# Optimization experiments

Measured on AMD Instinct MI355X. Metric: run time of the kernel, lower is better.

## Reference

```python
import jax, jax.numpy as jnp
import numpy as np

B, C, L, CH, CW = 2, 8, 512, 256, 8
NH = 8
FEATURES = 256
ROT = FEATURES // NH  # 32, partial rotary dim


def _rope(x, rot_dim):
    # x: (..., l, hd); rotate first rot_dim dims (interleaved pairs), pass rest through
    l = x.shape[-2]
    inv_freq = 1.0 / (10000.0 ** (jnp.arange(0, rot_dim, 2, dtype=jnp.float32) / rot_dim))
    freqs = jnp.arange(l, dtype=jnp.float32)[:, None] * inv_freq[None, :]  # (l, rot/2)
    freqs = jnp.repeat(freqs, 2, axis=-1)  # (l, rot)
    cos, sin = jnp.cos(freqs), jnp.sin(freqs)
    xr, xp = x[..., :rot_dim], x[..., rot_dim:]
    x2 = xr.reshape(xr.shape[:-1] + (rot_dim // 2, 2))
    rot = jnp.stack((-x2[..., 1], x2[..., 0]), axis=-1).reshape(xr.shape)
    return jnp.concatenate([xr * cos + rot * sin, xp], axis=-1)


def _conv(z, w):
    return jax.lax.conv_general_dilated(z, w, (1, 1), ((1, 1), (1, 1)),
                                        dimension_numbers=('NCHW', 'OIHW', 'NCHW'))


def _mlin(z, w):
    # per-channel linear over the height (features) axis: (n,c,h,w) x (c,g,h) -> (n,c,g,w)
    return jnp.einsum('nchw,cgh->ncgw', z, w)


def setup_inputs() -> dict:
    key = jax.random.key(0)
    ks = jax.random.split(key, 10)
    s_conv = 1.0 / np.sqrt(C * 9)
    s_lin = 1.0 / np.sqrt(FEATURES)
    return {
        'x': jax.random.normal(ks[0], (B, C, L, CH, CW), jnp.float32),
        'prev_qk': jax.random.normal(ks[1], (B, C, NH, L, L), jnp.float32),
        'conv_q_w': jax.random.normal(ks[2], (C, C, 3, 3), jnp.float32) * s_conv,
        'conv_k_w': jax.random.normal(ks[3], (C, C, 3, 3), jnp.float32) * s_conv,
        'conv_v_w': jax.random.normal(ks[4], (C, C, 3, 3), jnp.float32) * s_conv,
        'wq': jax.random.normal(ks[5], (C, FEATURES, FEATURES), jnp.float32) * s_lin,
        'wk': jax.random.normal(ks[6], (C, FEATURES, FEATURES), jnp.float32) * s_lin,
        'wv': jax.random.normal(ks[7], (C, FEATURES, FEATURES), jnp.float32) * s_lin,
        'wo': jax.random.normal(ks[8], (C, FEATURES, FEATURES), jnp.float32) * s_lin,
    }


def reference(x, prev_qk, conv_q_w, conv_k_w, conv_v_w, wq, wk, wv, wo):
    b, c, l, ch, cw = x.shape
    h = x.transpose(0, 2, 1, 3, 4).reshape(b * l, c, ch, cw)

    def heads(z):  # (b*l,c,ch,cw) -> (b,c,NH,l,hd)
        return (z.reshape(b, l, c, ch * cw).transpose(0, 2, 1, 3)
                 .reshape(b, c, l, NH, -1).transpose(0, 1, 3, 2, 4))

    q = heads(_mlin(_conv(h, conv_q_w), wq))
    k = heads(_mlin(_conv(h, conv_k_w), wk))
    v = heads(_mlin(_conv(h, conv_v_w), wv))

    q = _rope(q, ROT)
    k = _rope(k, ROT)

    qk = jnp.einsum('bcnld,bcnmd->bcnlm', q, k) / jnp.sqrt(jnp.float32(ch)) + prev_qk
    a = jnp.einsum('bcnlm,bcnmd->bcnld', jax.nn.softmax(qk, axis=-1), v)
    a = a.transpose(0, 1, 3, 2, 4).reshape(b, c, l, ch, cw)

    out = (_mlin(a.transpose(0, 2, 1, 3, 4).reshape(b * l, c, ch, cw), wo)
           .reshape(b, l, c, ch, cw).transpose(0, 2, 1, 3, 4))
    return out, qk
```

## Files before the change

### kernel.cpp

```cpp
#include <hip/hip_runtime.h>
#include <cstddef>
#include <cstdint>


typedef unsigned short u16;
typedef unsigned int u32;
typedef __attribute__((ext_vector_type(8))) short short8;
typedef __attribute__((ext_vector_type(4))) float floatx4;

__device__ __forceinline__ float bf2f(u16 u) {
  union { u32 i; float f; } v; v.i = ((u32)u) << 16; return v.f;
}
__device__ __forceinline__ u16 f2bf(float f) {
  union { float f; u32 i; } v; v.f = f;
  return (u16)((v.i + 0x7fffu + ((v.i >> 16) & 1u)) >> 16);
}

__global__ __launch_bounds__(256) void convert_w_kernel(
    const float* __restrict__ wq, const float* __restrict__ wk,
    const float* __restrict__ wv, const float* __restrict__ wo,
    u16* __restrict__ wbf) {
  int mat = blockIdx.y;
  const float* src = (mat == 0) ? wq : (mat == 1) ? wk : (mat == 2) ? wv : wo;
  int idx = blockIdx.x * 256 + threadIdx.x;
  wbf[(size_t)mat * 524288 + idx] = f2bf(src[idx]);
}

__global__ __launch_bounds__(256) void conv_fused_kernel(
    const float* __restrict__ x,
    const float* __restrict__ wq, const float* __restrict__ wk,
    const float* __restrict__ wv,
    u16* __restrict__ oq, u16* __restrict__ ok, u16* __restrict__ ov) {
  __shared__ float wl[1728];
  int t = threadIdx.x;
  for (int i2 = t; i2 < 1728; i2 += 256)
    wl[i2] = (i2 < 576) ? wq[i2] : (i2 < 1152 ? wk[i2 - 576] : wv[i2 - 1152]);
  __syncthreads();

  int bl = blockIdx.x >> 1, ih = blockIdx.x & 1;
  int b = bl >> 9, l = bl & 511;
  int il = t & 127, sh = t >> 7;
  int i = ih * 128 + il;

  float acc[12][8];
#pragma unroll
  for (int p = 0; p < 12; ++p)
#pragma unroll
    for (int j = 0; j < 8; ++j) acc[p][j] = 0.f;

  for (int ci = 0; ci < 8; ++ci) {
    const float* xc = x + (((size_t)(b * 8 + ci) * 512 + l) << 11);
    float xr[3][10];
#pragma unroll
    for (int di = 0; di < 3; ++di) {
      int gi = i + di - 1;
      xr[di][0] = 0.f; xr[di][9] = 0.f;
      if (gi >= 0 && gi < 256) {
        float4 a = *(const float4*)(xc + gi * 8);
        float4 bq = *(const float4*)(xc + gi * 8 + 4);
        xr[di][1] = a.x; xr[di][2] = a.y; xr[di][3] = a.z; xr[di][4] = a.w;
        xr[di][5] = bq.x; xr[di][6] = bq.y; xr[di][7] = bq.z; xr[di][8] = bq.w;
      } else {
#pragma unroll
        for (int j = 1; j < 9; ++j) xr[di][j] = 0.f;
      }
    }
#pragma unroll
    for (int p = 0; p < 12; ++p) {
      int pp = sh * 12 + p;
      int s = pp >> 3, co = pp & 7;
      const float* wp = &wl[s * 576 + (co * 8 + ci) * 9];
      float w00 = wp[0], w01 = wp[1], w02 = wp[2];
      float w10 = wp[3], w11 = wp[4], w12 = wp[5];
      float w20 = wp[6], w21 = wp[7], w22 = wp[8];
#pragma unroll
      for (int j = 0; j < 8; ++j) {
        acc[p][j] += w00 * xr[0][j] + w01 * xr[0][j + 1] + w02 * xr[0][j + 2]
                   + w10 * xr[1][j] + w11 * xr[1][j + 1] + w12 * xr[1][j + 2]
                   + w20 * xr[2][j] + w21 * xr[2][j + 1] + w22 * xr[2][j + 2];
      }
    }
  }
#pragma unroll
  for (int p = 0; p < 12; ++p) {
    int pp = sh * 12 + p;
    int s = pp >> 3, co = pp & 7;
    u16* ob = (s == 0) ? oq : (s == 1) ? ok : ov;
    size_t base = ((size_t)(bl * 8 + co)) << 11;
#pragma unroll
    for (int j = 0; j < 8; ++j) ob[base + j * 256 + i] = f2bf(acc[p][j]);
  }
}

template <int MODE>
__global__ __launch_bounds__(256) void mlin_mfma_kernel(
    const u16* __restrict__ zin,
    const u16* __restrict__ wbf,
    void* __restrict__ outp) {
  __shared__ u16 lds_a[8192];
  __shared__ u16 lds_b[8192];

  int tid = threadIdx.x;
  int wv = tid >> 6, lane = tid & 63;
  int fn = lane & 15, fq = lane >> 4;
  int wr = wv & 1, wc = wv >> 1;

  int bx = blockIdx.x;
  int c = bx >> 7;
  int cblk = (bx >> 1) & 63;
  int gblk = bx & 1;
  int g0 = gblk * 128;
  int col0 = cblk * 128;

  const u16* wsrc = wbf + ((size_t)c << 16);

  floatx4 acc[4][4];
#pragma unroll
  for (int mf = 0; mf < 4; ++mf)
#pragma unroll
    for (int nf = 0; nf < 4; ++nf) acc[mf][nf] = (floatx4){0.f, 0.f, 0.f, 0.f};

  for (int kt = 0; kt < 4; ++kt) {
    int h0 = kt * 64;
#pragma unroll
    for (int it = 0; it < 4; ++it) {
      int li = it * 256 + tid;
      int rr = li >> 3, hs = li & 7;
      uint4 ua = *(const uint4*)(wsrc + (size_t)(g0 + rr) * 256 + h0 + hs * 8);
      *(uint4*)((char*)lds_a + rr * 128 + ((hs ^ (rr & 7)) << 4)) = ua;
      uint4 ub = *(const uint4*)(zin +
          ((size_t)((cblk * 16 + (rr >> 3)) * 8 + c) << 11) + (rr & 7) * 256 +
          h0 + hs * 8);
      *(uint4*)((char*)lds_b + rr * 128 + ((hs ^ (rr & 7)) << 4)) = ub;
    }
    __syncthreads();
#pragma unroll
    for (int kc = 0; kc < 2; ++kc) {
      short8 af[4], bf[4];
#pragma unroll
      for (int mf = 0; mf < 4; ++mf) {
        int row = wr * 64 + mf * 16 + fn;
        af[mf] = *(const short8*)((const char*)lds_a + row * 128 +
                                  (((kc * 4 + fq) ^ (row & 7)) << 4));
      }
#pragma unroll
      for (int nf = 0; nf < 4; ++nf) {
        int row = wc * 64 + nf * 16 + fn;
        bf[nf] = *(const short8*)((const char*)lds_b + row * 128 +
                                  (((kc * 4 + fq) ^ (row & 7)) << 4));
      }
#pragma unroll
      for (int mf = 0; mf < 4; ++mf)
#pragma unroll
        for (int nf = 0; nf < 4; ++nf)
          acc[mf][nf] = __builtin_amdgcn_mfma_f32_16x16x32_bf16(
              af[mf], bf[nf], acc[mf][nf], 0, 0, 0);
    }
    __syncthreads();
  }

  if (MODE == 2) {
    float* op = (float*)outp;
#pragma unroll
    for (int nf = 0; nf < 4; ++nf) {
      int col = col0 + wc * 64 + nf * 16 + fn;
      int bl = col >> 3, w = col & 7;
      int b = bl >> 9, l = bl & 511;
      size_t rowoff = ((size_t)((b * 8 + c) * 512 + l) << 11) + w;
#pragma unroll
      for (int mf = 0; mf < 4; ++mf)
#pragma unroll
        for (int r = 0; r < 4; ++r) {
          int g = g0 + wr * 64 + mf * 16 + fq * 4 + r;
          op[rowoff + g * 8] = acc[mf][nf][r];
        }
    }
  } else {
    u16* op = (u16*)outp;
#pragma unroll
    for (int nf = 0; nf < 4; ++nf) {
      int col = col0 + wc * 64 + nf * 16 + fn;
      int bl = col >> 3, w = col & 7;
      int b = bl >> 9, l = bl & 511;
      size_t base = ((size_t)((b * 8 + c) * 8) << 17) + ((size_t)l << 8);
#pragma unroll
      for (int mf = 0; mf < 4; ++mf)
#pragma unroll
        for (int r = 0; r < 4; ++r) {
          int g = g0 + wr * 64 + mf * 16 + fq * 4 + r;
          float val = acc[mf][nf][r];
          if (MODE == 0) {
            float other = __shfl_xor(val, 1);
            int d = ((g & 31) << 3) + w;
            if (d < 32) {
              int p = d >> 1;
              float ang = (float)l * __expf(-(float)p * 0.57564627324851142f);
              float cv = cosf(ang), sv = sinf(ang);
              val = (d & 1) ? (val * cv + other * sv) : (val * cv - other * sv);
            }
          }
          int n = g >> 5, d2 = ((g & 31) << 3) + w;
          op[base + ((size_t)n << 17) + d2] = f2bf(val);
        }
    }
  }
}

__global__ __launch_bounds__(256) void transpose_v_kernel(const u16* __restrict__ vb,
                                                          u16* __restrict__ vt) {
  __shared__ u16 tile[64 * 66];
  int bx = blockIdx.x;
  int head = bx >> 5, mt = (bx >> 2) & 7, dt = bx & 3;
  size_t off = (size_t)head << 17;
  int t = threadIdx.x;
#pragma unroll
  for (int it = 0; it < 2; ++it) {
    int li = it * 256 + t;
    int r = li >> 3, cs = li & 7;
    uint4 u = *(const uint4*)(vb + off + (size_t)(mt * 64 + r) * 256 + dt * 64 + cs * 8);
    *(u32*)&tile[r * 66 + cs * 8 + 0] = u.x;
    *(u32*)&tile[r * 66 + cs * 8 + 2] = u.y;
    *(u32*)&tile[r * 66 + cs * 8 + 4] = u.z;
    *(u32*)&tile[r * 66 + cs * 8 + 6] = u.w;
  }
  __syncthreads();
#pragma unroll
  for (int it = 0; it < 2; ++it) {
    int li = it * 256 + t;
    int r = li >> 3, cs = li & 7;
    u16 tmp[8];
#pragma unroll
    for (int jj = 0; jj < 8; ++jj) tmp[jj] = tile[(cs * 8 + jj) * 66 + r];
    uint4 o;
    o.x = (u32)tmp[0] | ((u32)tmp[1] << 16);
    o.y = (u32)tmp[2] | ((u32)tmp[3] << 16);
    o.z = (u32)tmp[4] | ((u32)tmp[5] << 16);
    o.w = (u32)tmp[6] | ((u32)tmp[7] << 16);
    *(uint4*)(vt + off + (size_t)(dt * 64 + r) * 512 + mt * 64 + cs * 8) = o;
  }
}

__global__ __launch_bounds__(256) void attn_kernel(
    const u16* __restrict__ q, const u16* __restrict__ k,
    const u16* __restrict__ vt, const float* __restrict__ prev,
    float* __restrict__ qk_out, u16* __restrict__ a2) {
  __shared__ u16 s_bf[32 * 520];
  __shared__ u16 kv[32 * 288];
  __shared__ float rinv[32];

  int head = blockIdx.x >> 4;
  int l0 = (blockIdx.x & 15) << 5;
  int b = head >> 6, c = (head >> 3) & 7, nh = head & 7;
  size_t qoff = (size_t)head << 17;
  size_t poff = (size_t)head << 18;
  int tid = threadIdx.x;
  int w = tid >> 6, lane = tid & 63;
  int fn = lane & 15, fq = lane >> 4;
  int rt = w & 1, ct = w >> 1;

  short8 qf[8];
  const u16* qrow = q + qoff + (size_t)(l0 + rt * 16 + fn) * 256 + fq * 8;
#pragma unroll
  for (int kc = 0; kc < 8; ++kc) qf[kc] = *(const short8*)(qrow + kc * 32);

  for (int mc = 0; mc < 16; ++mc) {
    int m0 = mc * 32;
#pragma unroll
    for (int it = 0; it < 4; ++it) {
      int li = it * 256 + tid;
      int m = li >> 5, ds = li & 31;
      *(uint4*)&kv[m * 288 + ds * 8] =
          *(const uint4*)(k + qoff + (size_t)(m0 + m) * 256 + ds * 8);
    }
    __syncthreads();
    floatx4 acc = {0.f, 0.f, 0.f, 0.f};
    const u16* krow = &kv[(ct * 16 + fn) * 288 + fq * 8];
#pragma unroll
    for (int kc = 0; kc < 8; ++kc) {
      short8 bfr = *(const short8*)(krow + kc * 32);
      acc = __builtin_amdgcn_mfma_f32_16x16x32_bf16(qf[kc], bfr, acc, 0, 0, 0);
    }
#pragma unroll
    for (int r = 0; r < 4; ++r) {
      int lrow = rt * 16 + fq * 4 + r;
      int mcol = m0 + ct * 16 + fn;
      size_t gi = poff + (size_t)(l0 + lrow) * 512 + mcol;
      float sv = acc[r] * 0.0625f + prev[gi];
      qk_out[gi] = sv;
      s_bf[lrow * 520 + mcol] = f2bf(sv);
    }
    __syncthreads();
  }

  {
    int srow = tid >> 3, sseg = tid & 7;
    u16* sp = &s_bf[srow * 520 + sseg * 64];
    float mx = -1e30f;
#pragma unroll
    for (int ii = 0; ii < 8; ++ii) {
      uint4 u = *(const uint4*)(sp + ii * 8);
      mx = fmaxf(mx, fmaxf(fmaxf(fmaxf(bf2f(u.x & 0xffff), bf2f(u.x >> 16)),
                                 fmaxf(bf2f(u.y & 0xffff), bf2f(u.y >> 16))),
                           fmaxf(fmaxf(bf2f(u.z & 0xffff), bf2f(u.z >> 16)),
                                 fmaxf(bf2f(u.w & 0xffff), bf2f(u.w >> 16)))));
    }
#pragma unroll
    for (int o = 1; o < 8; o <<= 1) mx = fmaxf(mx, __shfl_xor(mx, o));
    float sum = 0.f;
#pragma unroll
    for (int ii = 0; ii < 8; ++ii) {
      uint4 u = *(const uint4*)(sp + ii * 8);
      float e0 = __expf(bf2f(u.x & 0xffff) - mx), e1 = __expf(bf2f(u.x >> 16) - mx);
      float e2 = __expf(bf2f(u.y & 0xffff) - mx), e3 = __expf(bf2f(u.y >> 16) - mx);
      float e4 = __expf(bf2f(u.z & 0xffff) - mx), e5 = __expf(bf2f(u.z >> 16) - mx);
      float e6 = __expf(bf2f(u.w & 0xffff) - mx), e7 = __expf(bf2f(u.w >> 16) - mx);
      sum += e0 + e1 + e2 + e3 + e4 + e5 + e6 + e7;
      uint4 o;
      o.x = (u32)f2bf(e0) | ((u32)f2bf(e1) << 16);
      o.y = (u32)f2bf(e2) | ((u32)f2bf(e3) << 16);
      o.z = (u32)f2bf(e4) | ((u32)f2bf(e5) << 16);
      o.w = (u32)f2bf(e6) | ((u32)f2bf(e7) << 16);
      *(uint4*)(sp + ii * 8) = o;
    }
#pragma unroll
    for (int o = 1; o < 8; o <<= 1) sum += __shfl_xor(sum, o);
    if (sseg == 0) rinv[srow] = 1.0f / sum;
  }

  floatx4 oacc[8];
#pragma unroll
  for (int dt = 0; dt < 8; ++dt) oacc[dt] = (floatx4){0.f, 0.f, 0.f, 0.f};

  for (int mc = 0; mc < 16; ++mc) {
    int m0 = mc * 32;
#pragma unroll
    for (int it = 0; it < 4; ++it) {
      int li = it * 256 + tid;
      int d = li >> 2, ms = li & 3;
      *(uint4*)&kv[d * 32 + ms * 8] =
          *(const uint4*)(vt + qoff + (size_t)d * 512 + m0 + ms * 8);
    }
    __syncthreads();
    short8 af = *(const short8*)&s_bf[(rt * 16 + fn) * 520 + m0 + fq * 8];
#pragma unroll
    for (int dt = 0; dt < 8; ++dt) {
      int d0 = ct * 128 + dt * 16;
      short8 bfr = *(const short8*)&kv[(d0 + fn) * 32 + fq * 8];
      oacc[dt] = __builtin_amdgcn_mfma_f32_16x16x32_bf16(af, bfr, oacc[dt], 0, 0, 0);
    }
    __syncthreads();
  }

  float riv[4];
#pragma unroll
  for (int r = 0; r < 4; ++r) riv[r] = rinv[rt * 16 + fq * 4 + r];
#pragma unroll
  for (int dt = 0; dt < 8; ++dt) {
#pragma unroll
    for (int r = 0; r < 4; ++r) {
      int lrow = l0 + rt * 16 + fq * 4 + r;
      int d = ct * 128 + dt * 16 + fn;
      int bl = b * 512 + lrow;
      a2[(size_t)(bl * 8 + c) * 2048 + ((d & 7) << 8) + (nh << 5) + (d >> 3)] =
          f2bf(oacc[dt][r] * riv[r]);
    }
  }
}

extern "C" void kernel_launch(void* const* d_in, const int* in_sizes, int n_in,
                              void* d_out, int out_size, void* d_ws, size_t ws_size,
                              hipStream_t stream) {
  const float* x    = (const float*)d_in[0];
  const float* prev = (const float*)d_in[1];
  const float* cqw  = (const float*)d_in[2];
  const float* ckw  = (const float*)d_in[3];
  const float* cvw  = (const float*)d_in[4];
  const float* wq   = (const float*)d_in[5];
  const float* wk   = (const float*)d_in[6];
  const float* wv   = (const float*)d_in[7];
  const float* wo   = (const float*)d_in[8];

  float* out    = (float*)d_out;
  float* qk_out = out + 16777216;

  char* wsb = (char*)d_ws;
  u16* wbf    = (u16*)wsb;
  u16* convq  = (u16*)(wsb + 8388608);
  u16* convk  = convq + 16777216;
  u16* convv  = convk + 16777216;
  u16* qb     = convv + 16777216;
  u16* kb     = qb + 16777216;
  u16* vb     = kb + 16777216;
  u16* vtb    = vb + 16777216;
  u16* a2     = vtb + 16777216;

  convert_w_kernel<<<dim3(2048, 4), 256, 0, stream>>>(wq, wk, wv, wo, wbf);
  conv_fused_kernel<<<2048, 256, 0, stream>>>(x, cqw, ckw, cvw, convq, convk, convv);
  mlin_mfma_kernel<0><<<1024, 256, 0, stream>>>(convq, wbf, qb);
  mlin_mfma_kernel<0><<<1024, 256, 0, stream>>>(convk, wbf + 524288, kb);
  mlin_mfma_kernel<1><<<1024, 256, 0, stream>>>(convv, wbf + 1048576, vb);
  transpose_v_kernel<<<4096, 256, 0, stream>>>(vb, vtb);
  attn_kernel<<<2048, 256, 0, stream>>>(qb, kb, vtb, prev, qk_out, a2);
  mlin_mfma_kernel<2><<<1024, 256, 0, stream>>>(a2, wbf + 1572864, out);
}
```

Baseline: 698.6 us.

## Load K/V MFMA fragments directly from global, drop LDS staging and barriers

The attention kernel no longer stages K and V^T tiles through shared memory. Each lane loads its MFMA B-fragments straight from global memory, which removes the per-iteration __syncthreads and the kv buffer. The change also remaps block indices so that consecutive blocks spread across heads, reorders softmax LDS reads to a strided pattern, sets launch bounds for 4 blocks per CU, and unrolls the loops by 2. The trade-off is more redundant global/L2 traffic, since the two row-tile waves each load the same K/V fragments, in exchange for fewer barriers and higher occupancy.

```diff
diff --git a/kernel.cpp b/kernel.cpp
--- a/kernel.cpp
+++ b/kernel.cpp
@@ -240,16 +240,17 @@
   }
 }
 
-__global__ __launch_bounds__(256) void attn_kernel(
+__global__ __launch_bounds__(256, 4) void attn_kernel(
     const u16* __restrict__ q, const u16* __restrict__ k,
     const u16* __restrict__ vt, const float* __restrict__ prev,
     float* __restrict__ qk_out, u16* __restrict__ a2) {
   __shared__ u16 s_bf[32 * 520];
-  __shared__ u16 kv[32 * 288];
   __shared__ float rinv[32];
 
-  int head = blockIdx.x >> 4;
-  int l0 = (blockIdx.x & 15) << 5;
+  int bx = blockIdx.x;
+  int bid = (bx & 7) * 256 + (bx >> 3);
+  int head = bid >> 4;
+  int l0 = (bid & 15) << 5;
   int b = head >> 6, c = (head >> 3) & 7, nh = head & 7;
   size_t qoff = (size_t)head << 17;
   size_t poff = (size_t)head << 18;
@@ -263,42 +264,39 @@
 #pragma unroll
   for (int kc = 0; kc < 8; ++kc) qf[kc] = *(const short8*)(qrow + kc * 32);
 
+  const u16* kbase = k + qoff + (size_t)(ct * 16 + fn) * 256 + fq * 8;
+  const float* prow = prev + poff + (size_t)(l0 + rt * 16 + fq * 4) * 512 + ct * 16 + fn;
+  float* qrow_out = qk_out + poff + (size_t)(l0 + rt * 16 + fq * 4) * 512 + ct * 16 + fn;
+#pragma unroll 2
   for (int mc = 0; mc < 16; ++mc) {
     int m0 = mc * 32;
-#pragma unroll
-    for (int it = 0; it < 4; ++it) {
-      int li = it * 256 + tid;
-      int m = li >> 5, ds = li & 31;
-      *(uint4*)&kv[m * 288 + ds * 8] =
-          *(const uint4*)(k + qoff + (size_t)(m0 + m) * 256 + ds * 8);
-    }
-    __syncthreads();
+    const u16* kr = kbase + ((size_t)m0 << 8);
+    short8 bfr[8];
+#pragma unroll
+    for (int kc = 0; kc < 8; ++kc) bfr[kc] = *(const short8*)(kr + kc * 32);
     floatx4 acc = {0.f, 0.f, 0.f, 0.f};
-    const u16* krow = &kv[(ct * 16 + fn) * 288 + fq * 8];
-#pragma unroll
-    for (int kc = 0; kc < 8; ++kc) {
-      short8 bfr = *(const short8*)(krow + kc * 32);
-      acc = __builtin_amdgcn_mfma_f32_16x16x32_bf16(qf[kc], bfr, acc, 0, 0, 0);
-    }
+#pragma unroll
+    for (int kc = 0; kc < 8; ++kc)
+      acc = __builtin_amdgcn_mfma_f32_16x16x32_bf16(qf[kc], bfr[kc], acc, 0, 0, 0);
+    float pv[4];
+#pragma unroll
+    for (int r = 0; r < 4; ++r) pv[r] = prow[(size_t)r * 512 + m0];
 #pragma unroll
     for (int r = 0; r < 4; ++r) {
-      int lrow = rt * 16 + fq * 4 + r;
-      int mcol = m0 + ct * 16 + fn;
-      size_t gi = poff + (size_t)(l0 + lrow) * 512 + mcol;
-      float sv = acc[r] * 0.0625f + prev[gi];
-      qk_out[gi] = sv;
-      s_bf[lrow * 520 + mcol] = f2bf(sv);
-    }
-    __syncthreads();
-  }
+      float sv = acc[r] * 0.0625f + pv[r];
+      qrow_out[(size_t)r * 512 + m0] = sv;
+      s_bf[(rt * 16 + fq * 4 + r) * 520 + m0 + ct * 16 + fn] = f2bf(sv);
+    }
+  }
+  __syncthreads();
 
   {
     int srow = tid >> 3, sseg = tid & 7;
-    u16* sp = &s_bf[srow * 520 + sseg * 64];
+    u16* sp = &s_bf[srow * 520 + sseg * 8];
     float mx = -1e30f;
 #pragma unroll
     for (int ii = 0; ii < 8; ++ii) {
-      uint4 u = *(const uint4*)(sp + ii * 8);
+      uint4 u = *(const uint4*)(sp + ii * 64);
       mx = fmaxf(mx, fmaxf(fmaxf(fmaxf(bf2f(u.x & 0xffff), bf2f(u.x >> 16)),
                                  fmaxf(bf2f(u.y & 0xffff), bf2f(u.y >> 16))),
                            fmaxf(fmaxf(bf2f(u.z & 0xffff), bf2f(u.z >> 16)),
@@ -309,7 +307,7 @@
     float sum = 0.f;
 #pragma unroll
     for (int ii = 0; ii < 8; ++ii) {
-      uint4 u = *(const uint4*)(sp + ii * 8);
+      uint4 u = *(const uint4*)(sp + ii * 64);
       float e0 = __expf(bf2f(u.x & 0xffff) - mx), e1 = __expf(bf2f(u.x >> 16) - mx);
       float e2 = __expf(bf2f(u.y & 0xffff) - mx), e3 = __expf(bf2f(u.y >> 16) - mx);
       float e4 = __expf(bf2f(u.z & 0xffff) - mx), e5 = __expf(bf2f(u.z >> 16) - mx);
@@ -320,35 +318,31 @@
       o.y = (u32)f2bf(e2) | ((u32)f2bf(e3) << 16);
       o.z = (u32)f2bf(e4) | ((u32)f2bf(e5) << 16);
       o.w = (u32)f2bf(e6) | ((u32)f2bf(e7) << 16);
-      *(uint4*)(sp + ii * 8) = o;
+      *(uint4*)(sp + ii * 64) = o;
     }
 #pragma unroll
     for (int o = 1; o < 8; o <<= 1) sum += __shfl_xor(sum, o);
     if (sseg == 0) rinv[srow] = 1.0f / sum;
   }
+  __syncthreads();
 
   floatx4 oacc[8];
 #pragma unroll
   for (int dt = 0; dt < 8; ++dt) oacc[dt] = (floatx4){0.f, 0.f, 0.f, 0.f};
 
+  const u16* vbase = vt + qoff + (size_t)(ct * 128 + fn) * 512 + fq * 8;
+  const u16* arow = &s_bf[(rt * 16 + fn) * 520 + fq * 8];
+#pragma unroll 2
   for (int mc = 0; mc < 16; ++mc) {
     int m0 = mc * 32;
-#pragma unroll
-    for (int it = 0; it < 4; ++it) {
-      int li = it * 256 + tid;
-      int d = li >> 2, ms = li & 3;
-      *(uint4*)&kv[d * 32 + ms * 8] =
-          *(const uint4*)(vt + qoff + (size_t)d * 512 + m0 + ms * 8);
-    }
-    __syncthreads();
-    short8 af = *(const short8*)&s_bf[(rt * 16 + fn) * 520 + m0 + fq * 8];
-#pragma unroll
-    for (int dt = 0; dt < 8; ++dt) {
-      int d0 = ct * 128 + dt * 16;
-      short8 bfr = *(const short8*)&kv[(d0 + fn) * 32 + fq * 8];
-      oacc[dt] = __builtin_amdgcn_mfma_f32_16x16x32_bf16(af, bfr, oacc[dt], 0, 0, 0);
-    }
-    __syncthreads();
+    short8 af = *(const short8*)(arow + m0);
+    short8 bfr[8];
+#pragma unroll
+    for (int dt = 0; dt < 8; ++dt)
+      bfr[dt] = *(const short8*)(vbase + (size_t)dt * 16 * 512 + m0);
+#pragma unroll
+    for (int dt = 0; dt < 8; ++dt)
+      oacc[dt] = __builtin_amdgcn_mfma_f32_16x16x32_bf16(af, bfr[dt], oacc[dt], 0, 0, 0);
   }
 
   float riv[4];
```

Measured after the change: 812.9 us. 16.4% more time.
